# Kernel optimization log

Measured on AMD Instinct MI355X. Metric: run time of the kernel, lower is better.

Reference implementation:

```python
import jax, jax.numpy as jnp
import numpy as np

NEG = -1e9  # large negative instead of -inf for numerical safety; masked rows are zeroed afterwards
LN_EPS = 1e-5


def layer_norm(x, g, b):
    mu = jnp.mean(x, axis=-1, keepdims=True)
    var = jnp.mean(jnp.square(x - mu), axis=-1, keepdims=True)
    return (x - mu) * jax.lax.rsqrt(var + LN_EPS) * g + b


def causal_conv1d(x_bct, w_oik):
    # x: [B, C, T], w: [O, I, K]; left-pad by K-1 (causal ConvNorm)
    k = w_oik.shape[-1]
    return jax.lax.conv_general_dilated(
        x_bct, w_oik, window_strides=(1,), padding=[(k - 1, 0)],
        dimension_numbers=('NCH', 'OIH', 'NCH'))


def setup_inputs() -> dict:
    key = jax.random.key(0)
    ks = jax.random.split(key, 8)
    B, T, D, H, F, K = 2, 2048, 1024, 16, 4096, 3
    MAXLEN = 4096
    x = jax.random.normal(ks[0], (B, T, D), dtype=jnp.float32)
    lengths = jnp.array([2048, 1536])
    x_mask = jnp.arange(T)[None, :] >= lengths[:, None]  # True = padded
    std = 0.02
    pos_table = jax.random.normal(ks[1], (MAXLEN, D), dtype=jnp.float32) * std
    w_qkv = jax.random.normal(ks[2], (3 * D, D), dtype=jnp.float32) * std
    w_o = jax.random.normal(ks[3], (D, D), dtype=jnp.float32) * std
    conv1_w = jax.random.normal(ks[4], (F, D, K), dtype=jnp.float32) * std
    conv2_w = jax.random.normal(ks[5], (D, F, K), dtype=jnp.float32) * std
    return {
        'x': x, 'x_mask': x_mask, 'pos_table': pos_table,
        'w_qkv': w_qkv, 'w_o': w_o,
        'ln1_g': jnp.ones((D,)), 'ln1_b': jnp.zeros((D,)),
        'ln2_g': jnp.ones((D,)), 'ln2_b': jnp.zeros((D,)),
        'conv1_w': conv1_w, 'conv2_w': conv2_w,
    }


def reference(x, x_mask, pos_table, w_qkv, w_o, ln1_g, ln1_b, ln2_g, ln2_b, conv1_w, conv2_w):
    B, T, D = x.shape
    H = 16
    dh = D // H
    scale = dh ** -0.5

    # ---- self-attention block (pre-norm) ----
    q_in = layer_norm(x, ln1_g, ln1_b)
    q_in = q_in + pos_table[:T][None]  # learnable positional embeddings
    qkv = jnp.einsum('btd,ed->bte', q_in, w_qkv).reshape(B, T, 3, H, dh)
    q, k, v = qkv[:, :, 0], qkv[:, :, 1], qkv[:, :, 2]
    scores = jnp.einsum('bthd,bshd->bhts', q, k) * scale  # [B,H,T,T]
    pad_mask = x_mask[:, None, :, None]                    # mask padded query rows
    causal = jnp.tril(jnp.ones((T, T), dtype=bool))[None, None]
    scores = jnp.where(pad_mask | ~causal, NEG, scores)
    prob = jax.nn.softmax(scores, axis=-1)
    prob = jnp.where(pad_mask, 0.0, prob)
    y = jnp.einsum('bhts,bshd->bthd', prob, v).reshape(B, T, D)
    y = jnp.einsum('btd,ed->bte', y, w_o)
    x = x + y  # dropout p=0

    # ---- positionwise causal conv FFN (pre-norm) ----
    h = layer_norm(x, ln2_g, ln2_b)
    h = jnp.transpose(h, (0, 2, 1))           # [B, D, T]
    h = causal_conv1d(h, conv1_w)             # [B, F, T]
    h = jax.nn.gelu(h, approximate=True)
    h = causal_conv1d(h, conv2_w)             # [B, D, T]
    h = jnp.transpose(h, (0, 2, 1))
    x = x + h
    return x
```

## Files before the change

kernel.cpp:

```cpp
#include <hip/hip_runtime.h>
#include <stdint.h>
#include <math.h>

#define T_SEQ 2048
#define D_MODEL 1024
#define NHEAD 16
#define DH 64
#define F_FF 4096
#define TP (T_SEQ + 2)

typedef unsigned short u16;
typedef float f32x4 __attribute__((ext_vector_type(4)));
typedef __bf16 bf16x8 __attribute__((ext_vector_type(8)));

__device__ __forceinline__ u16 f2bf(float f){
  unsigned u = __float_as_uint(f);
  u = u + 0x7fffu + ((u >> 16) & 1u);
  return (u16)(u >> 16);
}
__device__ __forceinline__ float b2f(u16 h){ return __uint_as_float(((unsigned)h) << 16); }

__device__ __forceinline__ float gelu_f(float x){
  const float c = 0.7978845608028654f;
  float u = c * (x + 0.044715f * x * x * x);
  float e = __expf(-2.0f * u);
  return x * __builtin_amdgcn_rcpf(1.0f + e);
}

#define AS1 __attribute__((address_space(1)))
#define AS3 __attribute__((address_space(3)))
__device__ __forceinline__ void async_cp16(void* lds, const void* g){
  __builtin_amdgcn_global_load_lds((AS1 void*)(void*)g, (AS3 void*)lds, 16, 0, 0);
}

__device__ __forceinline__ float fload(const void* p, size_t i, unsigned isbf){
  return isbf ? b2f(((const u16*)p)[i]) : ((const float*)p)[i];
}

__global__ void detect_dtype(const u16* __restrict__ x, unsigned* __restrict__ flags){
  unsigned e = ((unsigned)x[threadIdx.x] >> 7) & 0xFF;
  bool good = (e == 0 || (e >= 90 && e <= 150));
  unsigned long long b = __ballot(good);
  if (threadIdx.x == 0) flags[0] = (b == ~0ULL) ? 1u : 0u;
}

__global__ __launch_bounds__(256) void canon_mask(const unsigned char* __restrict__ raw,
                                                  unsigned char* __restrict__ canon){
  int i = blockIdx.x * 256 + threadIdx.x;
  if (i >= 2 * T_SEQ) return;
  unsigned char v;
  if (raw[3584]) {
    v = raw[i] != 0;
  } else if (raw[7168]) {
    v = ((const u16*)raw)[i] != 0;
  } else if (raw[14336]) {
    v = ((const int*)raw)[i] != 0;
  } else {
    v = ((const long long*)raw)[i] != 0;
  }
  canon[i] = v;
}

__global__ __launch_bounds__(256)
void cast_any2bf(const void* __restrict__ in, u16* __restrict__ out, int n,
                 const unsigned* __restrict__ flags){
  int i = (blockIdx.x * 256 + threadIdx.x) * 4;
  if (i >= n) return;
  if (flags[0]){
    *(ushort4*)(out + i) = *(const ushort4*)((const u16*)in + i);
  } else {
    float4 v = *(const float4*)((const float*)in + i);
    ushort4 o = { f2bf(v.x), f2bf(v.y), f2bf(v.z), f2bf(v.w) };
    *(ushort4*)(out + i) = o;
  }
}

__global__ __launch_bounds__(256)
void cast_out(const float* __restrict__ in, const float* __restrict__ res,
              void* __restrict__ out, int n, const unsigned* __restrict__ flags){
  int i = (blockIdx.x * 256 + threadIdx.x) * 4;
  if (i >= n) return;
  float4 v = *(const float4*)(in + i);
  float4 r = *(const float4*)(res + i);
  v.x += r.x; v.y += r.y; v.z += r.z; v.w += r.w;
  if (flags[0]){
    ushort4 o = { f2bf(v.x), f2bf(v.y), f2bf(v.z), f2bf(v.w) };
    *(ushort4*)((u16*)out + i) = o;
  } else {
    *(float4*)((float*)out + i) = v;
  }
}

template<int INX1>
__global__ __launch_bounds__(256)
void ln_kernel(const void* __restrict__ inv, const void* __restrict__ g,
               const void* __restrict__ be, const void* __restrict__ pos,
               u16* __restrict__ out, int addpos, int padout,
               const unsigned* __restrict__ flags)
{
  const unsigned isbf = flags[0];
  const int r = blockIdx.x;
  const int bb = r >> 11, tt = r & (T_SEQ - 1);
  const size_t ib = (size_t)r * D_MODEL + threadIdx.x * 4;
  float v0, v1, v2, v3;
  if (INX1){
    float4 v = *(const float4*)((const float*)inv + ib);
    v0 = v.x; v1 = v.y; v2 = v.z; v3 = v.w;
  } else if (isbf){
    ushort4 u = *(const ushort4*)((const u16*)inv + ib);
    v0 = b2f(u.x); v1 = b2f(u.y); v2 = b2f(u.z); v3 = b2f(u.w);
  } else {
    float4 v = *(const float4*)((const float*)inv + ib);
    v0 = v.x; v1 = v.y; v2 = v.z; v3 = v.w;
  }
  float s  = v0 + v1 + v2 + v3;
  float s2 = v0*v0 + v1*v1 + v2*v2 + v3*v3;
  #pragma unroll
  for (int o = 1; o < 64; o <<= 1){ s += __shfl_xor(s, o); s2 += __shfl_xor(s2, o); }
  __shared__ float w1[4], w2[4];
  int w = threadIdx.x >> 6;
  if ((threadIdx.x & 63) == 0){ w1[w] = s; w2[w] = s2; }
  __syncthreads();
  float S  = w1[0] + w1[1] + w1[2] + w1[3];
  float S2 = w2[0] + w2[1] + w2[2] + w2[3];
  float mu  = S * (1.f / 1024.f);
  float var = S2 * (1.f / 1024.f) - mu * mu;
  float rs  = rsqrtf(var + 1e-5f);
  int d0 = threadIdx.x * 4;
  float o0 = (v0 - mu) * rs * fload(g, d0 + 0, isbf) + fload(be, d0 + 0, isbf);
  float o1 = (v1 - mu) * rs * fload(g, d0 + 1, isbf) + fload(be, d0 + 1, isbf);
  float o2 = (v2 - mu) * rs * fload(g, d0 + 2, isbf) + fload(be, d0 + 2, isbf);
  float o3 = (v3 - mu) * rs * fload(g, d0 + 3, isbf) + fload(be, d0 + 3, isbf);
  if (addpos){
    size_t pb = (size_t)tt * D_MODEL + d0;
    o0 += fload(pos, pb + 0, isbf);
    o1 += fload(pos, pb + 1, isbf);
    o2 += fload(pos, pb + 2, isbf);
    o3 += fload(pos, pb + 3, isbf);
  }
  size_t orow = padout ? ((size_t)bb * TP + tt + 2) * (size_t)D_MODEL
                       : (size_t)r * D_MODEL;
  ushort4 ov = { f2bf(o0), f2bf(o1), f2bf(o2), f2bf(o3) };
  *(ushort4*)(out + orow + d0) = ov;
}

__global__ __launch_bounds__(256)
void conv_w_split(const void* __restrict__ in, u16* __restrict__ out, int lg2C,
                  const unsigned* __restrict__ flags){
  int i = blockIdx.x * 256 + threadIdx.x;
  if (i >= 4096 * 1024) return;
  const unsigned isbf = flags[0];
  const int C = 1 << lg2C;
  int c = i & (C - 1);
  size_t sb = (size_t)i * 3;
  size_t ob = (size_t)(i >> lg2C) * 3 * C + c;
  out[ob]         = f2bf(fload(in, sb + 0, isbf));
  out[ob + C]     = f2bf(fload(in, sb + 1, isbf));
  out[ob + 2 * C] = f2bf(fload(in, sb + 2, isbf));
}

__global__ __launch_bounds__(256)
void zero_pads(u16* __restrict__ h2pad, u16* __restrict__ g1pad){
  int tid = blockIdx.x * 256 + threadIdx.x;
  if (tid < 2 * 2 * D_MODEL){
    int b = tid >> 11; int off = tid & (2 * D_MODEL - 1);
    h2pad[(size_t)b * TP * D_MODEL + off] = 0;
  }
  if (tid < 2 * 2 * F_FF){
    int b = tid >> 13; int off = tid & (2 * F_FF - 1);
    g1pad[(size_t)b * TP * F_FF + off] = 0;
  }
}

__device__ __forceinline__ int swz(int tid){
  return (tid & 3) ^ ((tid >> 2) & 3) ^ ((tid >> 4) & 3);
}

template<int MODE>
__global__ __launch_bounds__(256)
void gemm_bt(const u16* __restrict__ A, const u16* __restrict__ B,
             const void* __restrict__ res, void* __restrict__ outp,
             int N, int Kin, int lg2Kin, int nseg, long Abstride,
             const unsigned* __restrict__ flags)
{
  __shared__ u16 smA[128 * 32];
  __shared__ u16 smB[128 * 32];
  const int tid = threadIdx.x;
  const int m0 = blockIdx.y * 128;
  const int n0 = blockIdx.x * 128;
  const int Ktot = Kin * nseg;

  const int ch = swz(tid);
  long abase[2]; const u16* bbase[2];
  #pragma unroll
  for (int i = 0; i < 2; ++i){
    int r = m0 + i * 64 + (tid >> 2);
    int bb = r >> 11, tt = r & (T_SEQ - 1);
    abase[i] = (long)bb * Abstride + (long)tt * Kin + ch * 8;
    bbase[i] = B + (long)(n0 + i * 64 + (tid >> 2)) * Ktot + ch * 8;
  }

  f32x4 acc[4][4];
  #pragma unroll
  for (int i = 0; i < 4; ++i)
    #pragma unroll
    for (int j = 0; j < 4; ++j){ f32x4 z = {0.f,0.f,0.f,0.f}; acc[i][j] = z; }

  const int wm = (tid >> 6) & 1, wn = (tid >> 7) & 1;
  const int lane = tid & 63, lq = lane >> 4, lr = lane & 15;
  const int xq = lq ^ (lr & 3) ^ (lr >> 2);
  const int aoff = (wm * 64 + lr) * 32 + xq * 8;
  const int boff = (wn * 64 + lr) * 32 + xq * 8;

  for (int k0 = 0; k0 < Ktot; k0 += 32){
    int seg = k0 >> lg2Kin;
    int j0  = k0 & (Kin - 1);
    long aso = (long)seg * Kin + j0;
    long bso = k0;
    #pragma unroll
    for (int i = 0; i < 2; ++i){
      async_cp16(&smA[i * 2048 + tid * 8], A + abase[i] + aso);
      async_cp16(&smB[i * 2048 + tid * 8], bbase[i] + bso);
    }
    __syncthreads();
    bf16x8 af[4], bfv[4];
    #pragma unroll
    for (int mi = 0; mi < 4; ++mi) af[mi]  = *(const bf16x8*)&smA[aoff + mi * 512];
    #pragma unroll
    for (int ni = 0; ni < 4; ++ni) bfv[ni] = *(const bf16x8*)&smB[boff + ni * 512];
    #pragma unroll
    for (int mi = 0; mi < 4; ++mi)
      #pragma unroll
      for (int ni = 0; ni < 4; ++ni)
        acc[mi][ni] = __builtin_amdgcn_mfma_f32_16x16x32_bf16(af[mi], bfv[ni], acc[mi][ni], 0, 0, 0);
    __syncthreads();
  }

  const unsigned isbf = (MODE == 1 || MODE == 3) ? flags[0] : 0;
  #pragma unroll
  for (int mi = 0; mi < 4; ++mi){
    #pragma unroll
    for (int ni = 0; ni < 4; ++ni){
      int row0 = m0 + wm * 64 + mi * 16 + lq * 4;
      int col  = n0 + wn * 64 + ni * 16 + lr;
      if (MODE == 0){
        ushort4 pv = { f2bf(acc[mi][ni][0]), f2bf(acc[mi][ni][1]),
                       f2bf(acc[mi][ni][2]), f2bf(acc[mi][ni][3]) };
        if (col < 2 * D_MODEL){
          #pragma unroll
          for (int rr = 0; rr < 4; ++rr)
            ((u16*)outp)[(size_t)(row0 + rr) * N + col] = ((const u16*)&pv)[rr];
        } else {
          int hh = (col - 2 * D_MODEL) >> 6, dd = (col - 2 * D_MODEL) & 63;
          int bb = row0 >> 11, tt = row0 & (T_SEQ - 1);
          *(ushort4*)((u16*)const_cast<void*>(res) +
                      ((size_t)(bb * NHEAD + hh) * 64 + dd) * T_SEQ + tt) = pv;
        }
      } else {
        #pragma unroll
        for (int rr = 0; rr < 4; ++rr){
          int row = row0 + rr;
          float v = acc[mi][ni][rr];
          size_t idx = (size_t)row * N + col;
          if (MODE == 1){
            ((float*)outp)[idx] = v + fload(res, idx, isbf);
          } else if (MODE == 3){
            float ov = v + ((const float*)res)[idx];
            if (isbf) ((u16*)outp)[idx] = f2bf(ov);
            else      ((float*)outp)[idx] = ov;
          }
        }
      }
    }
  }
}

__device__ __forceinline__ void ktile8(
    f32x4 (&acc)[8][4], u16 (*L)[16384], int buf, int abase, int bbase,
    const u16* __restrict__ A, const long (&asrc)[2], const u16* const (&bsrc)[2],
    const int (&adst)[2], const int (&bdst)[2], int kt, bool stage_ok)
{
  const u16* Lp = L[buf];
  u16* Ld = L[(kt + 3) & 3];
  bf16x8 bfr[4], a0[4], a1[4];
  #pragma unroll
  for (int nf = 0; nf < 4; ++nf) bfr[nf] = *(const bf16x8*)&Lp[bbase + nf * 512];
  #pragma unroll
  for (int j = 0; j < 4; ++j) a0[j] = *(const bf16x8*)&Lp[abase + j * 512];
  if (stage_ok){
    #pragma unroll
    for (int s = 0; s < 2; ++s)
      async_cp16(&Ld[adst[s]], A + asrc[s] + (long)(kt + 3) * 32);
  }
  #pragma unroll
  for (int j = 0; j < 4; ++j) a1[j] = *(const bf16x8*)&Lp[abase + (4 + j) * 512];
  if (stage_ok){
    #pragma unroll
    for (int s = 0; s < 2; ++s)
      async_cp16(&Ld[bdst[s]], bsrc[s] + (long)(kt + 3) * 32);
  }
  __builtin_amdgcn_s_setprio(1);
  #pragma unroll
  for (int j = 0; j < 4; ++j)
    #pragma unroll
    for (int nf = 0; nf < 4; ++nf)
      acc[j][nf] = __builtin_amdgcn_mfma_f32_16x16x32_bf16(a0[j], bfr[nf], acc[j][nf], 0, 0, 0);
  #pragma unroll
  for (int j = 0; j < 4; ++j)
    #pragma unroll
    for (int nf = 0; nf < 4; ++nf)
      acc[4 + j][nf] = __builtin_amdgcn_mfma_f32_16x16x32_bf16(a1[j], bfr[nf], acc[4 + j][nf], 0, 0, 0);
  __builtin_amdgcn_s_setprio(0);
}

template<int MODE>
__global__ __launch_bounds__(512, 2)
void gemm8(const u16* __restrict__ A, const u16* __restrict__ Bm,
           void* __restrict__ outp, int N, int Kin, int Ktot, int nkt, long Abstride)
{
  __shared__ u16 L[4][16384];
  const int tid = threadIdx.x;
  const int m0 = blockIdx.y * 256, n0 = blockIdx.x * 256;
  const int kt0 = (MODE == 4) ? blockIdx.z * nkt : 0;
  const int ktEnd = kt0 + nkt;

  const int rl = tid >> 2;
  const int ch = swz(tid);
  long asrc[2]; const u16* bsrc[2]; int adst[2], bdst[2];
  #pragma unroll
  for (int s = 0; s < 2; ++s){
    int r = m0 + s * 128 + rl;
    int bb = r >> 11, tt = r & (T_SEQ - 1);
    asrc[s] = (long)bb * Abstride + (long)tt * Kin + ch * 8;
    bsrc[s] = Bm + (long)(n0 + s * 128 + rl) * Ktot + ch * 8;
    adst[s] = (s * 512 + tid) * 8;
    bdst[s] = 8192 + adst[s];
  }

  const int w = tid >> 6, lane = tid & 63;
  const int wm = w >> 2, wn = w & 3;
  const int quad = lane >> 4, lr = lane & 15;
  const int xq = quad ^ (lr & 3) ^ (lr >> 2);
  const int abase = ((wm * 128 + lr) * 4 + xq) * 8;
  const int bbase = 8192 + ((wn * 64 + lr) * 4 + xq) * 8;

  f32x4 acc[8][4];
  #pragma unroll
  for (int i = 0; i < 8; ++i)
    #pragma unroll
    for (int j = 0; j < 4; ++j){ f32x4 z = {0.f,0.f,0.f,0.f}; acc[i][j] = z; }

  #pragma unroll
  for (int j = 0; j < 3; ++j){
    #pragma unroll
    for (int s = 0; s < 2; ++s) async_cp16(&L[(kt0 + j) & 3][adst[s]], A + asrc[s] + (long)(kt0 + j) * 32);
    #pragma unroll
    for (int s = 0; s < 2; ++s) async_cp16(&L[(kt0 + j) & 3][bdst[s]], bsrc[s] + (long)(kt0 + j) * 32);
  }

  int kt = kt0;
  for (; kt < ktEnd - 2; ++kt){
    asm volatile("s_waitcnt vmcnt(8)" ::: "memory");
    __builtin_amdgcn_s_barrier();
    __builtin_amdgcn_sched_barrier(0);
    ktile8(acc, L, kt & 3, abase, bbase, A, asrc, bsrc, adst, bdst, kt, kt + 3 < ktEnd);
  }
  asm volatile("s_waitcnt vmcnt(4)" ::: "memory");
  __builtin_amdgcn_s_barrier();
  __builtin_amdgcn_sched_barrier(0);
  ktile8(acc, L, (ktEnd - 2) & 3, abase, bbase, A, asrc, bsrc, adst, bdst, ktEnd - 2, false);
  asm volatile("s_waitcnt vmcnt(0)" ::: "memory");
  __builtin_amdgcn_s_barrier();
  __builtin_amdgcn_sched_barrier(0);
  ktile8(acc, L, (ktEnd - 1) & 3, abase, bbase, A, asrc, bsrc, adst, bdst, ktEnd - 1, false);

  #pragma unroll
  for (int mf = 0; mf < 8; ++mf){
    #pragma unroll
    for (int nf = 0; nf < 4; ++nf){
      int col = n0 + wn * 64 + nf * 16 + lr;
      #pragma unroll
      for (int rr = 0; rr < 4; ++rr){
        int row = m0 + wm * 128 + mf * 16 + quad * 4 + rr;
        if (MODE == 2){
          int bb = row >> 11, tt = row & (T_SEQ - 1);
          ((u16*)outp)[((size_t)(bb * TP + tt + 2)) * N + col] = f2bf(gelu_f(acc[mf][nf][rr]));
        } else {
          atomicAdd((float*)outp + (size_t)row * N + col, acc[mf][nf][rr]);
        }
      }
    }
  }
}

__global__ __launch_bounds__(256)
void attn_mfma(const u16* __restrict__ qkv, const u16* __restrict__ vT,
               const unsigned char* __restrict__ mask, u16* __restrict__ y)
{
  const int qb = blockIdx.x, h = blockIdx.y, b = blockIdx.z;
  const int q0 = qb * 64;
  const int tid = threadIdx.x;

  if (mask[b * T_SEQ + q0]){
    int r = tid >> 2, c4 = (tid & 3) * 16;
    u16* yp = y + (size_t)(b * T_SEQ + q0 + r) * D_MODEL + h * DH + c4;
    ushort4 z = {0, 0, 0, 0};
    #pragma unroll
    for (int c = 0; c < 4; ++c) *(ushort4*)(yp + c * 4) = z;
    return;
  }

  const int w = tid >> 6, lane = tid & 63;
  const int quad = lane >> 4, lr = lane & 15;

  __shared__ u16 Ks[64 * 72];
  __shared__ u16 Vs[64 * 72];
  __shared__ u16 Ps[64 * 72];

  bf16x8 aq0, aq1;
  {
    const u16* qp = qkv + (size_t)(b * T_SEQ + q0 + w * 16 + lr) * 3072 + h * DH + quad * 8;
    aq0 = *(const bf16x8*)qp;
    aq1 = *(const bf16x8*)(qp + 32);
  }

  f32x4 acc_o[4];
  #pragma unroll
  for (int i = 0; i < 4; ++i){ f32x4 z = {0.f,0.f,0.f,0.f}; acc_o[i] = z; }
  float mrow[4] = {-1e30f, -1e30f, -1e30f, -1e30f};
  float lrow[4] = {0.f, 0.f, 0.f, 0.f};

  const int sr = tid >> 3, sg = tid & 7;

  for (int it = 0; it <= qb; ++it){
    const int s0 = it * 64;
    #pragma unroll
    for (int rr = 0; rr < 64; rr += 32){
      int row = sr + rr;
      *(uint4*)&Ks[row * 72 + sg * 8] =
        *(const uint4*)(qkv + (size_t)(b * T_SEQ + s0 + row) * 3072 + D_MODEL + h * DH + sg * 8);
      *(uint4*)&Vs[row * 72 + sg * 8] =
        *(const uint4*)(vT + ((size_t)(b * NHEAD + h) * 64 + row) * T_SEQ + s0 + sg * 8);
    }
    __syncthreads();

    f32x4 accs[4];
    #pragma unroll
    for (int nt = 0; nt < 4; ++nt){
      f32x4 z = {0.f, 0.f, 0.f, 0.f};
      bf16x8 bk0 = *(const bf16x8*)&Ks[(nt * 16 + lr) * 72 + quad * 8];
      bf16x8 bk1 = *(const bf16x8*)&Ks[(nt * 16 + lr) * 72 + quad * 8 + 32];
      z = __builtin_amdgcn_mfma_f32_16x16x32_bf16(aq0, bk0, z, 0, 0, 0);
      z = __builtin_amdgcn_mfma_f32_16x16x32_bf16(aq1, bk1, z, 0, 0, 0);
      accs[nt] = z;
    }

    const bool diag = (it == qb);
    float sv[4][4], mx[4];
    #pragma unroll
    for (int rr = 0; rr < 4; ++rr) mx[rr] = -1e30f;
    #pragma unroll
    for (int nt = 0; nt < 4; ++nt){
      #pragma unroll
      for (int rr = 0; rr < 4; ++rr){
        float s = accs[nt][rr] * 0.125f;
        if (diag && (nt * 16 + lr) > (w * 16 + quad * 4 + rr)) s = -1e30f;
        sv[nt][rr] = s;
        mx[rr] = fmaxf(mx[rr], s);
      }
    }
    #pragma unroll
    for (int o = 1; o < 16; o <<= 1){
      #pragma unroll
      for (int rr = 0; rr < 4; ++rr) mx[rr] = fmaxf(mx[rr], __shfl_xor(mx[rr], o));
    }
    float alpha[4], psum[4];
    #pragma unroll
    for (int rr = 0; rr < 4; ++rr){
      float mnew = fmaxf(mrow[rr], mx[rr]);
      alpha[rr] = __expf(mrow[rr] - mnew);
      mrow[rr] = mnew;
      psum[rr] = 0.f;
    }
    #pragma unroll
    for (int nt = 0; nt < 4; ++nt){
      #pragma unroll
      for (int rr = 0; rr < 4; ++rr){
        float p = __expf(sv[nt][rr] - mrow[rr]);
        psum[rr] += p;
        Ps[(w * 16 + quad * 4 + rr) * 72 + nt * 16 + lr] = f2bf(p);
      }
    }
    #pragma unroll
    for (int o = 1; o < 16; o <<= 1){
      #pragma unroll
      for (int rr = 0; rr < 4; ++rr) psum[rr] += __shfl_xor(psum[rr], o);
    }
    #pragma unroll
    for (int rr = 0; rr < 4; ++rr) lrow[rr] = lrow[rr] * alpha[rr] + psum[rr];
    #pragma unroll
    for (int nt = 0; nt < 4; ++nt)
      #pragma unroll
      for (int rr = 0; rr < 4; ++rr) acc_o[nt][rr] *= alpha[rr];

    bf16x8 ap0 = *(const bf16x8*)&Ps[(w * 16 + lr) * 72 + quad * 8];
    bf16x8 ap1 = *(const bf16x8*)&Ps[(w * 16 + lr) * 72 + quad * 8 + 32];
    #pragma unroll
    for (int nt = 0; nt < 4; ++nt){
      bf16x8 bv0 = *(const bf16x8*)&Vs[(nt * 16 + lr) * 72 + quad * 8];
      bf16x8 bv1 = *(const bf16x8*)&Vs[(nt * 16 + lr) * 72 + quad * 8 + 32];
      acc_o[nt] = __builtin_amdgcn_mfma_f32_16x16x32_bf16(ap0, bv0, acc_o[nt], 0, 0, 0);
      acc_o[nt] = __builtin_amdgcn_mfma_f32_16x16x32_bf16(ap1, bv1, acc_o[nt], 0, 0, 0);
    }
    __syncthreads();
  }

  #pragma unroll
  for (int rr = 0; rr < 4; ++rr){
    int qg = q0 + w * 16 + quad * 4 + rr;
    float inv = 1.0f / lrow[rr];
    bool rm = mask[b * T_SEQ + qg] != 0;
    #pragma unroll
    for (int nt = 0; nt < 4; ++nt){
      float v = rm ? 0.f : acc_o[nt][rr] * inv;
      y[(size_t)(b * T_SEQ + qg) * D_MODEL + h * DH + nt * 16 + lr] = f2bf(v);
    }
  }
}

extern "C" void kernel_launch(void* const* d_in, const int* in_sizes, int n_in,
                              void* d_out, int out_size, void* d_ws, size_t ws_size,
                              hipStream_t stream)
{
  const void* x       = d_in[0];
  const unsigned char* xmask_raw = (const unsigned char*)d_in[1];
  const void* pos     = d_in[2];
  const void* w_qkv   = d_in[3];
  const void* w_o     = d_in[4];
  const void* ln1_g   = d_in[5];
  const void* ln1_b   = d_in[6];
  const void* ln2_g   = d_in[7];
  const void* ln2_b   = d_in[8];
  const void* conv1_w = d_in[9];
  const void* conv2_w = d_in[10];

  char* ws = (char*)d_ws;
  size_t o = 0;
  auto alloc = [&](size_t bytes){ size_t cur = o; o += (bytes + 255) & ~(size_t)255; return cur; };
  unsigned* flags = (unsigned*)(ws + alloc(256));
  unsigned char* maskc = (unsigned char*)(ws + alloc(2 * T_SEQ));
  float* x1   = (float*)(ws + alloc((size_t)2 * T_SEQ * D_MODEL * 4));
  char* h2slab = ws + alloc((size_t)2 * TP * D_MODEL * 2);
  u16* g1pad  = (u16*)(ws + alloc((size_t)2 * TP * F_FF * 2));
  u16* slabA  = (u16*)(ws + alloc((size_t)4096 * 3072 * 2));
  u16* qy     = (u16*)(ws + alloc((size_t)4096 * 1024 * 2));
  char* vslab = ws + alloc((size_t)4096 * 1024 * 4);
  u16* vt     = (u16*)vslab;
  float* xc   = (float*)vslab;

  u16* wqkv_c = (u16*)h2slab;
  u16* wo_c   = (u16*)h2slab + (size_t)3072 * 1024;
  u16* h2pad  = (u16*)h2slab;
  u16* qin    = qy;
  u16* qkvb   = slabA;
  u16* yb     = qy;
  u16* W1cat  = slabA;
  u16* W2cat  = slabA;

  detect_dtype<<<1, 64, 0, stream>>>((const u16*)x, flags);
  canon_mask<<<16, 256, 0, stream>>>(xmask_raw, maskc);
  cast_any2bf<<<3072 * 1024 / 4 / 256, 256, 0, stream>>>(w_qkv, wqkv_c, 3072 * 1024, flags);
  cast_any2bf<<<1024 * 1024 / 4 / 256, 256, 0, stream>>>(w_o, wo_c, 1024 * 1024, flags);
  ln_kernel<0><<<4096, 256, 0, stream>>>(x, ln1_g, ln1_b, pos, qin, 1, 0, flags);
  gemm_bt<0><<<dim3(24, 32), 256, 0, stream>>>(qin, wqkv_c, vt, qkvb,
                                               3072, 1024, 10, 1, (long)T_SEQ * 1024, flags);
  attn_mfma<<<dim3(32, 16, 2), 256, 0, stream>>>(qkvb, vt, maskc, yb);
  gemm_bt<1><<<dim3(8, 32), 256, 0, stream>>>(yb, wo_c, x, x1,
                                              1024, 1024, 10, 1, (long)T_SEQ * 1024, flags);
  hipMemsetAsync(xc, 0, (size_t)4096 * 1024 * 4, stream);
  conv_w_split<<<4096 * 1024 / 256, 256, 0, stream>>>(conv1_w, W1cat, 10, flags);
  zero_pads<<<64, 256, 0, stream>>>(h2pad, g1pad);
  ln_kernel<1><<<4096, 256, 0, stream>>>(x1, ln2_g, ln2_b, nullptr, h2pad, 0, 1, flags);
  gemm8<2><<<dim3(16, 16, 1), 512, 0, stream>>>(h2pad, W1cat, g1pad,
                                                4096, 1024, 3072, 96, (long)TP * 1024);
  conv_w_split<<<4096 * 1024 / 256, 256, 0, stream>>>(conv2_w, W2cat, 12, flags);
  gemm8<4><<<dim3(4, 16, 4), 512, 0, stream>>>(g1pad, W2cat, xc,
                                               1024, 4096, 12288, 96, (long)TP * 4096);
  cast_out<<<4096 * 1024 / 4 / 256, 256, 0, stream>>>(xc, x1, d_out, 4096 * 1024, flags);
}
```

Measured before the change: 644.9 us.

## Restructure FFN GEMM to BK=64 double-buffered pipeline with interleaved MFMA clusters

The conv FFN GEMM moves from a 4-stage ring of K=32 tiles to a 2-stage double buffer of K=64 tiles with separate A and B LDS arrays and a new XOR swizzle. Each k-tile is split into four MFMA clusters, each bracketed by barriers, and the global-to-LDS loads for the next tiles are interleaved between them. The aim is to halve loop iterations and barrier/wait overhead per unit of K while keeping loads hidden behind MFMA work. The extra barriers per cluster and the shallower prefetch depth could expose memory latency, and the loop assumes an even number of k-tiles.

```diff
diff --git a/kernel.cpp b/kernel.cpp
--- a/kernel.cpp
+++ b/kernel.cpp
@@ -275,74 +275,57 @@
   }
 }
 
-__device__ __forceinline__ void ktile8(
-    f32x4 (&acc)[8][4], u16 (*L)[16384], int buf, int abase, int bbase,
-    const u16* __restrict__ A, const long (&asrc)[2], const u16* const (&bsrc)[2],
-    const int (&adst)[2], const int (&bdst)[2], int kt, bool stage_ok)
-{
-  const u16* Lp = L[buf];
-  u16* Ld = L[(kt + 3) & 3];
-  bf16x8 bfr[4], a0[4], a1[4];
-  #pragma unroll
-  for (int nf = 0; nf < 4; ++nf) bfr[nf] = *(const bf16x8*)&Lp[bbase + nf * 512];
-  #pragma unroll
-  for (int j = 0; j < 4; ++j) a0[j] = *(const bf16x8*)&Lp[abase + j * 512];
-  if (stage_ok){
-    #pragma unroll
-    for (int s = 0; s < 2; ++s)
-      async_cp16(&Ld[adst[s]], A + asrc[s] + (long)(kt + 3) * 32);
-  }
-  #pragma unroll
-  for (int j = 0; j < 4; ++j) a1[j] = *(const bf16x8*)&Lp[abase + (4 + j) * 512];
-  if (stage_ok){
-    #pragma unroll
-    for (int s = 0; s < 2; ++s)
-      async_cp16(&Ld[bdst[s]], bsrc[s] + (long)(kt + 3) * 32);
-  }
-  __builtin_amdgcn_s_setprio(1);
-  #pragma unroll
-  for (int j = 0; j < 4; ++j)
-    #pragma unroll
-    for (int nf = 0; nf < 4; ++nf)
-      acc[j][nf] = __builtin_amdgcn_mfma_f32_16x16x32_bf16(a0[j], bfr[nf], acc[j][nf], 0, 0, 0);
-  #pragma unroll
-  for (int j = 0; j < 4; ++j)
-    #pragma unroll
-    for (int nf = 0; nf < 4; ++nf)
-      acc[4 + j][nf] = __builtin_amdgcn_mfma_f32_16x16x32_bf16(a1[j], bfr[nf], acc[4 + j][nf], 0, 0, 0);
-  __builtin_amdgcn_s_setprio(0);
-}
-
 template<int MODE>
 __global__ __launch_bounds__(512, 2)
 void gemm8(const u16* __restrict__ A, const u16* __restrict__ Bm,
            void* __restrict__ outp, int N, int Kin, int Ktot, int nkt, long Abstride)
 {
-  __shared__ u16 L[4][16384];
+  __shared__ u16 LA[2][16384];
+  __shared__ u16 LB[2][16384];
   const int tid = threadIdx.x;
   const int m0 = blockIdx.y * 256, n0 = blockIdx.x * 256;
   const int kt0 = (MODE == 4) ? blockIdx.z * nkt : 0;
   const int ktEnd = kt0 + nkt;
-
-  const int rl = tid >> 2;
-  const int ch = swz(tid);
-  long asrc[2]; const u16* bsrc[2]; int adst[2], bdst[2];
-  #pragma unroll
-  for (int s = 0; s < 2; ++s){
-    int r = m0 + s * 128 + rl;
-    int bb = r >> 11, tt = r & (T_SEQ - 1);
-    asrc[s] = (long)bb * Abstride + (long)tt * Kin + ch * 8;
-    bsrc[s] = Bm + (long)(n0 + s * 128 + rl) * Ktot + ch * 8;
-    adst[s] = (s * 512 + tid) * 8;
-    bdst[s] = 8192 + adst[s];
-  }
-
-  const int w = tid >> 6, lane = tid & 63;
+  const int w = tid >> 6, l = tid & 63;
   const int wm = w >> 2, wn = w & 3;
-  const int quad = lane >> 4, lr = lane & 15;
-  const int xq = quad ^ (lr & 3) ^ (lr >> 2);
-  const int abase = ((wm * 128 + lr) * 4 + xq) * 8;
-  const int bbase = 8192 + ((wn * 64 + lr) * 4 + xq) * 8;
+  const int quad = l >> 4, lr = l & 15;
+
+  const int chg = (l & 7) ^ (l >> 3);
+  int srcA[2][2], srcB[2][2], dst[2][2];
+  #pragma unroll
+  for (int h = 0; h < 2; ++h)
+    #pragma unroll
+    for (int j = 0; j < 2; ++j){
+      int row128 = (w * 2 + j) * 8 + (l >> 3);
+      int rA = m0 + h * 128 + row128;
+      int bb = rA >> 11, tt = rA & (T_SEQ - 1);
+      srcA[h][j] = bb * (int)Abstride + tt * Kin + chg * 8;
+      srcB[h][j] = (n0 + h * 128 + row128) * Ktot + chg * 8;
+      dst[h][j]  = h * 8192 + (w * 2 + j) * 512 + l * 8;
+    }
+
+  const int xq0 = quad ^ (lr & 7);
+
+  auto stageA = [&](int kt, int h, int bs){
+    long ko = (long)kt * 64;
+    #pragma unroll
+    for (int j = 0; j < 2; ++j)
+      async_cp16(&LA[bs][dst[h][j]], A + srcA[h][j] + ko);
+  };
+  auto stageB = [&](int kt, int h, int bs){
+    long ko = (long)kt * 64;
+    #pragma unroll
+    for (int j = 0; j < 2; ++j)
+      async_cp16(&LB[bs][dst[h][j]], Bm + srcB[h][j] + ko);
+  };
+  auto LDAf = [&](int bs, int mf, int ks) -> bf16x8 {
+    int row = wm * 128 + mf * 16 + lr;
+    return *(const bf16x8*)&LA[bs][row * 64 + ((xq0 ^ (ks << 2)) * 8)];
+  };
+  auto LDBf = [&](int bs, int nf, int ks) -> bf16x8 {
+    int row = wn * 64 + nf * 16 + lr;
+    return *(const bf16x8*)&LB[bs][row * 64 + ((xq0 ^ (ks << 2)) * 8)];
+  };
 
   f32x4 acc[8][4];
   #pragma unroll
@@ -350,29 +333,58 @@
     #pragma unroll
     for (int j = 0; j < 4; ++j){ f32x4 z = {0.f,0.f,0.f,0.f}; acc[i][j] = z; }
 
-  #pragma unroll
-  for (int j = 0; j < 3; ++j){
-    #pragma unroll
-    for (int s = 0; s < 2; ++s) async_cp16(&L[(kt0 + j) & 3][adst[s]], A + asrc[s] + (long)(kt0 + j) * 32);
-    #pragma unroll
-    for (int s = 0; s < 2; ++s) async_cp16(&L[(kt0 + j) & 3][bdst[s]], bsrc[s] + (long)(kt0 + j) * 32);
-  }
-
-  int kt = kt0;
-  for (; kt < ktEnd - 2; ++kt){
-    asm volatile("s_waitcnt vmcnt(8)" ::: "memory");
+  stageA(kt0, 0, 0); stageA(kt0, 1, 0); stageB(kt0, 0, 0); stageB(kt0, 1, 0);
+  stageA(kt0 + 1, 0, 1); stageA(kt0 + 1, 1, 1);
+
+#define MMCL(MFB, AR, BR)                                                     \
+  __builtin_amdgcn_s_barrier();                                               \
+  __builtin_amdgcn_sched_barrier(0);                                          \
+  __builtin_amdgcn_s_setprio(1);                                              \
+  _Pragma("unroll")                                                           \
+  for (int mi = 0; mi < 4; ++mi)                                              \
+    _Pragma("unroll")                                                         \
+    for (int nf = 0; nf < 4; ++nf)                                            \
+      acc[MFB + mi][nf] = __builtin_amdgcn_mfma_f32_16x16x32_bf16(            \
+          AR[mi], BR[nf], acc[MFB + mi][nf], 0, 0, 0);                        \
+  __builtin_amdgcn_s_setprio(0);                                              \
+  __builtin_amdgcn_s_barrier();                                               \
+  __builtin_amdgcn_sched_barrier(0);
+
+  auto HALF = [&](int bs, int Tt, bool drain){
+    if (drain) asm volatile("s_waitcnt vmcnt(0)" ::: "memory");
+    else       asm volatile("s_waitcnt vmcnt(4)" ::: "memory");
     __builtin_amdgcn_s_barrier();
     __builtin_amdgcn_sched_barrier(0);
-    ktile8(acc, L, kt & 3, abase, bbase, A, asrc, bsrc, adst, bdst, kt, kt + 3 < ktEnd);
-  }
-  asm volatile("s_waitcnt vmcnt(4)" ::: "memory");
-  __builtin_amdgcn_s_barrier();
-  __builtin_amdgcn_sched_barrier(0);
-  ktile8(acc, L, (ktEnd - 2) & 3, abase, bbase, A, asrc, bsrc, adst, bdst, ktEnd - 2, false);
-  asm volatile("s_waitcnt vmcnt(0)" ::: "memory");
-  __builtin_amdgcn_s_barrier();
-  __builtin_amdgcn_sched_barrier(0);
-  ktile8(acc, L, (ktEnd - 1) & 3, abase, bbase, A, asrc, bsrc, adst, bdst, ktEnd - 1, false);
+    bf16x8 a0[4], a1[4], a2[4], a3[4], b0[4], b1[4];
+    #pragma unroll
+    for (int i = 0; i < 4; ++i) a0[i] = LDAf(bs, i, 0);
+    #pragma unroll
+    for (int i = 0; i < 4; ++i) b0[i] = LDBf(bs, i, 0);
+    #pragma unroll
+    for (int i = 0; i < 4; ++i) a1[i] = LDAf(bs, i, 1);
+    if (Tt + 1 < ktEnd) stageB(Tt + 1, 0, bs ^ 1);
+    MMCL(0, a0, b0)
+    #pragma unroll
+    for (int i = 0; i < 4; ++i) a2[i] = LDAf(bs, 4 + i, 0);
+    #pragma unroll
+    for (int i = 0; i < 4; ++i) a3[i] = LDAf(bs, 4 + i, 1);
+    #pragma unroll
+    for (int i = 0; i < 4; ++i) b1[i] = LDBf(bs, i, 1);
+    if (Tt + 1 < ktEnd) stageB(Tt + 1, 1, bs ^ 1);
+    MMCL(4, a2, b0)
+    if (Tt + 2 < ktEnd) stageA(Tt + 2, 0, bs);
+    MMCL(0, a1, b1)
+    if (Tt + 2 < ktEnd) stageA(Tt + 2, 1, bs);
+    MMCL(4, a3, b1)
+  };
+
+  const int NI = nkt >> 1;
+  for (int it = 0; it < NI; ++it){
+    int T = kt0 + it * 2;
+    HALF(0, T, false);
+    HALF(1, T + 1, it == NI - 1);
+  }
+#undef MMCL
 
   #pragma unroll
   for (int mf = 0; mf < 8; ++mf){
@@ -582,9 +594,9 @@
   zero_pads<<<64, 256, 0, stream>>>(h2pad, g1pad);
   ln_kernel<1><<<4096, 256, 0, stream>>>(x1, ln2_g, ln2_b, nullptr, h2pad, 0, 1, flags);
   gemm8<2><<<dim3(16, 16, 1), 512, 0, stream>>>(h2pad, W1cat, g1pad,
-                                                4096, 1024, 3072, 96, (long)TP * 1024);
+                                                4096, 1024, 3072, 48, (long)TP * 1024);
   conv_w_split<<<4096 * 1024 / 256, 256, 0, stream>>>(conv2_w, W2cat, 12, flags);
   gemm8<4><<<dim3(4, 16, 4), 512, 0, stream>>>(g1pad, W2cat, xc,
-                                               1024, 4096, 12288, 96, (long)TP * 4096);
+                                               1024, 4096, 12288, 48, (long)TP * 4096);
   cast_out<<<4096 * 1024 / 4 / 256, 256, 0, stream>>>(xc, x1, d_out, 4096 * 1024, flags);
 }
```

Result: slower. 702.3 us (+8.9%).
